# Optimization experiments

Measured on AMD Instinct MI355X. Metric: run time of the kernel, lower is better.

Reference implementation:

```python
import jax, jax.numpy as jnp
import numpy as np

N_EMBED = 384
N_HEAD = 6
HEAD_SIZE = N_EMBED // N_HEAD  # 64
LN_EPS = 1e-5


def setup_inputs() -> dict:
    key = jax.random.key(0)
    ks = jax.random.split(key, 12)
    B, T = 128, 256
    s_in = 1.0 / np.sqrt(N_EMBED)
    s_ff = 1.0 / np.sqrt(4 * N_EMBED)
    return {
        "x": jax.random.normal(ks[0], (B, T, N_EMBED), jnp.float32),
        "Wq": jax.random.normal(ks[1], (N_HEAD, N_EMBED, HEAD_SIZE), jnp.float32) * s_in,
        "Wk": jax.random.normal(ks[2], (N_HEAD, N_EMBED, HEAD_SIZE), jnp.float32) * s_in,
        "Wv": jax.random.normal(ks[3], (N_HEAD, N_EMBED, HEAD_SIZE), jnp.float32) * s_in,
        "Wproj": jax.random.normal(ks[4], (N_EMBED, N_EMBED), jnp.float32) * s_in,
        "bproj": jnp.zeros((N_EMBED,), jnp.float32),
        "W1": jax.random.normal(ks[5], (N_EMBED, 4 * N_EMBED), jnp.float32) * s_in,
        "b1": jnp.zeros((4 * N_EMBED,), jnp.float32),
        "W2": jax.random.normal(ks[6], (4 * N_EMBED, N_EMBED), jnp.float32) * s_ff,
        "b2": jnp.zeros((N_EMBED,), jnp.float32),
        "ln1_g": jnp.ones((N_EMBED,), jnp.float32),
        "ln1_b": jnp.zeros((N_EMBED,), jnp.float32),
        "ln2_g": jnp.ones((N_EMBED,), jnp.float32),
        "ln2_b": jnp.zeros((N_EMBED,), jnp.float32),
    }


def _layernorm(x, g, b):
    mu = jnp.mean(x, axis=-1, keepdims=True)
    var = jnp.mean(jnp.square(x - mu), axis=-1, keepdims=True)
    return (x - mu) * jax.lax.rsqrt(var + LN_EPS) * g + b


def _attention(xn, Wq, Wk, Wv, Wproj, bproj):
    B, T, C = xn.shape
    q = jnp.einsum("btc,hcd->bhtd", xn, Wq)
    k = jnp.einsum("btc,hcd->bhtd", xn, Wk)
    v = jnp.einsum("btc,hcd->bhtd", xn, Wv)
    # NOTE: original scales by C**-0.5 with C = n_embed (384), not head_size
    scores = jnp.einsum("bhtd,bhsd->bhts", q, k) * (C ** -0.5)
    causal = jnp.tril(jnp.ones((T, T), bool))
    scores = jnp.where(causal, scores, -jnp.inf)
    wei = jax.nn.softmax(scores, axis=-1)
    out = jnp.einsum("bhts,bhsd->bhtd", wei, v)
    out = out.transpose(0, 2, 1, 3).reshape(B, T, N_EMBED)  # concat heads
    return out @ Wproj + bproj


def reference(x, Wq, Wk, Wv, Wproj, bproj, W1, b1, W2, b2, ln1_g, ln1_b, ln2_g, ln2_b):
    x = x + _attention(_layernorm(x, ln1_g, ln1_b), Wq, Wk, Wv, Wproj, bproj)
    h = _layernorm(x, ln2_g, ln2_b)
    ff = jax.nn.relu(h @ W1 + b1) @ W2 + b2
    return x + ff
```

## Files before the change

### kernel.cpp

```cpp
#include <hip/hip_runtime.h>
#include <hip/hip_bf16.h>

typedef __hip_bfloat16 bf16;
typedef __attribute__((ext_vector_type(8))) short bf16x8;
typedef __attribute__((ext_vector_type(4))) float f32x4;

#define CEMB 384
#define NHEAD 6
#define HSZ 64
#define TSEQ 256
#define BATCH 128
#define MROWS (BATCH*TSEQ)
#define FDIM 1536
#define QSCALE 0.05103103630798288f
#define SMAX 8.0f

#define AS1 __attribute__((address_space(1)))
#define AS3 __attribute__((address_space(3)))
__device__ __forceinline__ void gload16(const void* g, void* l){
  __builtin_amdgcn_global_load_lds((const AS1 unsigned*)(g), (AS3 unsigned*)(l), 16, 0, 0);
}

__global__ __launch_bounds__(256) void ln_kernel(const float* __restrict__ x,
    const float* __restrict__ gam, const float* __restrict__ bet,
    bf16* __restrict__ y)
{
  const int row  = blockIdx.x*4 + (threadIdx.x>>6);
  const int lane = threadIdx.x & 63;
  const float* xr = x + (size_t)row*CEMB;
  float v[6]; float s = 0.f;
  #pragma unroll
  for (int i=0;i<6;i++){ v[i] = xr[lane + i*64]; s += v[i]; }
  #pragma unroll
  for (int m=1;m<64;m<<=1) s += __shfl_xor(s, m, 64);
  const float mu = s * (1.0f/CEMB);
  float qs = 0.f;
  #pragma unroll
  for (int i=0;i<6;i++){ v[i] -= mu; qs += v[i]*v[i]; }
  #pragma unroll
  for (int m=1;m<64;m<<=1) qs += __shfl_xor(qs, m, 64);
  const float rs = rsqrtf(qs*(1.0f/CEMB) + 1e-5f);
  bf16* yr = y + (size_t)row*CEMB;
  #pragma unroll
  for (int i=0;i<6;i++){
    int c = lane + i*64;
    yr[c] = __float2bfloat16(v[i]*rs*gam[c] + bet[c]);
  }
}

__global__ __launch_bounds__(256) void transpose_to_bf16(const float* __restrict__ src,
    bf16* __restrict__ dst, int K, int N)
{
  __shared__ float tile[32][33];
  const int n0 = blockIdx.x*32, k0 = blockIdx.y*32;
  src += (size_t)blockIdx.z*K*N;
  dst += (size_t)blockIdx.z*K*N;
  const int c = threadIdx.x & 31, r8 = threadIdx.x >> 5;
  #pragma unroll
  for (int i=0;i<4;i++)
    tile[r8 + i*8][c] = src[(size_t)(k0 + r8 + i*8)*N + n0 + c];
  __syncthreads();
  #pragma unroll
  for (int i=0;i<4;i++)
    dst[(size_t)(n0 + r8 + i*8)*K + k0 + c] = __float2bfloat16(tile[c][r8 + i*8]);
}

__global__ __launch_bounds__(256) void transpose_qkv(const float* __restrict__ Wq,
    const float* __restrict__ Wk, const float* __restrict__ Wv, bf16* __restrict__ dst)
{
  __shared__ float tile[32][33];
  const int z = blockIdx.z;
  const float* src = (z < 6) ? Wq : (z < 12 ? Wk : Wv);
  src += (size_t)(z % 6) * CEMB * HSZ;
  dst += (size_t)z * CEMB * HSZ;
  const int n0 = blockIdx.x*32, k0 = blockIdx.y*32;
  const int c = threadIdx.x & 31, r8 = threadIdx.x >> 5;
  #pragma unroll
  for (int i=0;i<4;i++)
    tile[r8 + i*8][c] = src[(size_t)(k0 + r8 + i*8)*HSZ + n0 + c];
  __syncthreads();
  #pragma unroll
  for (int i=0;i<4;i++)
    dst[(size_t)(n0 + r8 + i*8)*CEMB + k0 + c] = __float2bfloat16(tile[c][r8 + i*8]);
}

template<int EPI, int NREAL, int NPAD, int NK>
__global__ __launch_bounds__(512, 2) void gemm8p(
    const bf16* __restrict__ A, const bf16* __restrict__ BT,
    const float* __restrict__ bias, const float* __restrict__ resid,
    float* __restrict__ outf, bf16* __restrict__ outb0,
    bf16* __restrict__ outb1, bf16* __restrict__ outb2)
{
  constexpr int K = NK*64;
  constexpr int NT = NPAD/256;
  __shared__ char lds[131072];
  const int cpx = gridDim.x >> 3;
  const int wg  = (blockIdx.x & 7)*cpx + (blockIdx.x >> 3);
  const int bm = (wg / NT)*256, bn = (wg % NT)*256;
  const int t = threadIdx.x, lane = t & 63, wid = t >> 6;
  const int wm = wid >> 2, wn = wid & 3;
  const int g = lane >> 4, fr = lane & 15;
  const size_t rowb = (size_t)K*2;
  const int sblk = ((t&3) ^ ((t>>3)&3)) << 4;
  const int swz  = (g ^ ((fr>>1)&3)) << 4;
  f32x4 acc[8][4] = {};

  const char* Ag = (const char*)A  + (size_t)(bm + (t>>2))*rowb + sblk;
  const char* Bg = (const char*)BT + (size_t)(bn + (t>>2))*rowb + sblk;
  const size_t rstep = rowb*128;

  auto stg = [&](int X, int KH, int sl, int kt2){
    const char* src = (X ? Bg : Ag) + (size_t)kt2*128 + KH*64;
    char* dst = lds + X*65536 + (KH*2+sl)*16384 + wid*1024;
    gload16(src,         dst);
    gload16(src + rstep, dst + 8192);
  };
  auto rdA = [&](bf16x8* af, int sl, int MH, int KS){
    const char* p = lds + (KS*2+sl)*16384 + (wm*128 + MH*64 + fr)*64 + swz;
    #pragma unroll
    for (int mi=0;mi<4;mi++) af[mi] = *(const bf16x8*)(p + mi*1024);
  };
  auto rdB = [&](bf16x8* bq, int sl, int KS){
    const char* p = lds + 65536 + (KS*2+sl)*16384 + (wn*64 + fr)*64 + swz;
    #pragma unroll
    for (int nj=0;nj<4;nj++) bq[nj] = *(const bf16x8*)(p + nj*1024);
  };

#define MFMA16(MH) \
  __builtin_amdgcn_s_setprio(1); \
  _Pragma("unroll") \
  for (int mi=0;mi<4;mi++){ \
    _Pragma("unroll") \
    for (int nj=0;nj<4;nj++) \
      acc[(MH)*4+mi][nj] = __builtin_amdgcn_mfma_f32_16x16x32_bf16(af[mi], bq[nj], acc[(MH)*4+mi][nj], 0, 0, 0); \
  } \
  __builtin_amdgcn_s_setprio(0);

  stg(0,0,0,0); stg(1,0,0,0); stg(0,1,0,0); stg(1,1,0,0);
  asm volatile("s_waitcnt vmcnt(4)" ::: "memory");
  __builtin_amdgcn_s_barrier();

  #pragma unroll 1
  for (int kt=0; kt<NK; ++kt){
    const int sl = kt&1, sn = sl^1;
    const bool pf = (kt+1 < NK);
    bf16x8 af[4], bq[4];
    rdA(af, sl, 0, 0); rdB(bq, sl, 0);
    if (pf) stg(0,0,sn,kt+1);
    __builtin_amdgcn_s_barrier();
    asm volatile("s_waitcnt lgkmcnt(0)" ::: "memory");
    __builtin_amdgcn_sched_barrier(0);
    MFMA16(0)
    __builtin_amdgcn_s_barrier();
    rdA(af, sl, 1, 0);
    if (pf){ stg(1,0,sn,kt+1);
             asm volatile("s_waitcnt vmcnt(4)" ::: "memory"); }
    else     asm volatile("s_waitcnt vmcnt(0)" ::: "memory");
    __builtin_amdgcn_s_barrier();
    asm volatile("s_waitcnt lgkmcnt(0)" ::: "memory");
    __builtin_amdgcn_sched_barrier(0);
    MFMA16(1)
    __builtin_amdgcn_s_barrier();
    rdA(af, sl, 0, 1); rdB(bq, sl, 1);
    if (pf) stg(0,1,sn,kt+1);
    __builtin_amdgcn_s_barrier();
    asm volatile("s_waitcnt lgkmcnt(0)" ::: "memory");
    __builtin_amdgcn_sched_barrier(0);
    MFMA16(0)
    __builtin_amdgcn_s_barrier();
    rdA(af, sl, 1, 1);
    if (pf){ stg(1,1,sn,kt+1);
             asm volatile("s_waitcnt vmcnt(4)" ::: "memory"); }
    __builtin_amdgcn_s_barrier();
    asm volatile("s_waitcnt lgkmcnt(0)" ::: "memory");
    __builtin_amdgcn_sched_barrier(0);
    MFMA16(1)
    __builtin_amdgcn_s_barrier();
  }
#undef MFMA16

  #pragma unroll
  for (int mi=0;mi<8;mi++)
    #pragma unroll
    for (int nj=0;nj<4;nj++)
      #pragma unroll
      for (int e=0;e<4;e++){
        const int m = bm + wm*128 + mi*16 + 4*g + e;
        const int n = bn + wn*64 + nj*16 + fr;
        if (NPAD == NREAL || n < NREAL){
          const float vacc = acc[mi][nj][e];
          if constexpr (EPI==0){
            int sel = n/CEMB; int nn = n - sel*CEMB;
            int hh = nn>>6, dd = nn&63;
            int bb = m>>8,  tt = m&255;
            bf16 val = __float2bfloat16(sel==0 ? vacc * QSCALE : vacc);
            bf16* dst = sel==0 ? outb0 : (sel==1 ? outb1 : outb2);
            dst[((size_t)(bb*NHEAD + hh)*TSEQ + tt)*HSZ + dd] = val;
          } else if constexpr (EPI==1){
            outf[(size_t)m*NREAL + n] = vacc + bias[n] + resid[(size_t)m*NREAL + n];
          } else {
            float z = vacc + bias[n];
            outb0[(size_t)m*NREAL + n] = __float2bfloat16(z > 0.f ? z : 0.f);
          }
        }
      }
}

template<int EPI, int NN, int NK>
__global__ __launch_bounds__(512) void gemm3(
    const bf16* __restrict__ A, const bf16* __restrict__ BT,
    const float* __restrict__ bias, const float* __restrict__ resid,
    float* __restrict__ outf)
{
  constexpr int K = NK*32;
  constexpr int N = NN*128;
  __shared__ char lA[2][256*64];
  __shared__ char lB[2][128*64];
  const int cpx = gridDim.x >> 3;
  const int wg  = (blockIdx.x & 7)*cpx + (blockIdx.x >> 3);
  const int bm = (wg / NN)*256, bn = (wg % NN)*128;
  const int t = threadIdx.x, lane = t & 63, wid = t >> 6;
  const int wr = (wid>>1)*64, wc = (wid&1)*64;
  const int g = lane >> 4, fr = lane & 15;
  const size_t rowK2 = (size_t)K*2;
  f32x4 acc[4][4] = {};

  auto stage = [&](int buf, int kt){
    const size_t ko = (size_t)kt*64;
    #pragma unroll
    for (int i=0;i<2;i++){
      int slot = t + i*512;
      int row = slot>>2, blk = slot&3;
      gload16((const char*)A + (size_t)(bm+row)*rowK2 + ko + ((blk ^ ((row>>1)&3))<<4),
              lA[buf] + slot*16);
    }
    {
      int row = t>>2, blk = t&3;
      gload16((const char*)BT + (size_t)(bn+row)*rowK2 + ko + ((blk ^ ((row>>1)&3))<<4),
              lB[buf] + t*16);
    }
  };

  stage(0, 0);
  __syncthreads();
  int cur = 0;
  #pragma unroll 1
  for (int kt=0; kt<NK; ++kt){
    if (kt+1 < NK) stage(cur^1, kt+1);
    bf16x8 af[4], bq[4];
    #pragma unroll
    for (int mi=0;mi<4;mi++){
      int row = wr + mi*16 + fr;
      af[mi] = *(const bf16x8*)(lA[cur] + row*64 + ((g ^ ((row>>1)&3))<<4));
    }
    #pragma unroll
    for (int nj=0;nj<4;nj++){
      int row = wc + nj*16 + fr;
      bq[nj] = *(const bf16x8*)(lB[cur] + row*64 + ((g ^ ((row>>1)&3))<<4));
    }
    __builtin_amdgcn_s_setprio(1);
    #pragma unroll
    for (int mi=0;mi<4;mi++)
      #pragma unroll
      for (int nj=0;nj<4;nj++)
        acc[mi][nj] = __builtin_amdgcn_mfma_f32_16x16x32_bf16(af[mi], bq[nj], acc[mi][nj], 0, 0, 0);
    __builtin_amdgcn_s_setprio(0);
    __syncthreads();
    cur ^= 1;
  }
  #pragma unroll
  for (int mi=0;mi<4;mi++)
    #pragma unroll
    for (int nj=0;nj<4;nj++)
      #pragma unroll
      for (int e=0;e<4;e++){
        const int m = bm + wr + mi*16 + 4*g + e;
        const int n = bn + wc + nj*16 + fr;
        outf[(size_t)m*N + n] = acc[mi][nj][e] + bias[n] + resid[(size_t)m*N + n];
      }
}

__global__ __launch_bounds__(256) void attn_kernel(
    const bf16* __restrict__ q, const bf16* __restrict__ k,
    const bf16* __restrict__ v, bf16* __restrict__ out)
{
  __shared__ char kt_lds[64*128];
  __shared__ char vt_lds[80*128];
  __shared__ char p_lds[4][64*128];
  const int bh = blockIdx.x;
  const int bidx = bh / NHEAD, hidx = bh - bidx*NHEAD;
  const int t = threadIdx.x, lane = t & 63, w = t >> 6;
  const int g = lane >> 4, fr = lane & 15;
  const int lrow = lane >> 3;
  const int scol = ((lane & 7) ^ lrow) << 4;
  const size_t base = (size_t)bh * TSEQ * HSZ;

  if (t < 128){
    unsigned int ones2 = 0x3F803F80u;
    uint4 vv;
    if ((t>>3) == 0) vv = uint4{ones2, ones2, ones2, ones2};
    else             vv = uint4{0u, 0u, 0u, 0u};
    *(uint4*)(vt_lds + (64 + (t>>3))*128 + (t&7)*16) = vv;
  }

  bf16x8 qf[4][2];
  #pragma unroll
  for (int mi=0;mi<4;mi++)
    #pragma unroll
    for (int ks=0;ks<2;ks++)
      qf[mi][ks] = *(const bf16x8*)(q + base + (size_t)(w*64 + mi*16 + fr)*HSZ + ks*32 + g*8);

  f32x4 of[4][5] = {};

  for (int j=0;j<4;j++){
    __syncthreads();
    #pragma unroll
    for (int i=0;i<2;i++){
      int r0 = w*16 + i*8;
      gload16((const char*)(k + base + (size_t)(j*64 + r0 + lrow)*HSZ) + scol,
              kt_lds + r0*128);
    }
    #pragma unroll
    for (int i=0;i<2;i++){
      int chunk = t + i*256, r = chunk>>3, c = chunk&7;
      uint4 vv = *(const uint4*)(v + base + (size_t)(j*64 + r)*HSZ + c*8);
      const unsigned short* pv = (const unsigned short*)&vv;
      #pragma unroll
      for (int u=0;u<8;u++)
        *(unsigned short*)(vt_lds + (c*8+u)*128 + ((((r>>3) ^ u ^ c)&7)<<4) + (r&7)*2) = pv[u];
    }
    __syncthreads();
    if (j <= w){
      f32x4 sa[4][4] = {};
      #pragma unroll
      for (int ks=0;ks<2;ks++){
        bf16x8 kf[4];
        #pragma unroll
        for (int nj=0;nj<4;nj++)
          kf[nj] = *(const bf16x8*)(kt_lds + (nj*16+fr)*128 + (((ks*4+g)*16) ^ ((fr&7)<<4)));
        __builtin_amdgcn_s_setprio(1);
        #pragma unroll
        for (int mi=0;mi<4;mi++)
          #pragma unroll
          for (int nj=0;nj<4;nj++)
            sa[mi][nj] = __builtin_amdgcn_mfma_f32_16x16x32_bf16(qf[mi][ks], kf[nj], sa[mi][nj], 0, 0, 0);
        __builtin_amdgcn_s_setprio(0);
      }
      if (j == w){
        #pragma unroll
        for (int mi=0;mi<4;mi++)
          #pragma unroll
          for (int nj=0;nj<4;nj++)
            #pragma unroll
            for (int e=0;e<4;e++)
              if (nj*16 + fr > mi*16 + 4*g + e) sa[mi][nj][e] = -1e30f;
      }
      char* pl = p_lds[w];
      #pragma unroll
      for (int mi=0;mi<4;mi++)
        #pragma unroll
        for (int nj=0;nj<4;nj++)
          #pragma unroll
          for (int e=0;e<4;e++){
            int row = mi*16 + 4*g + e, col = nj*16 + fr;
            float p = __expf(sa[mi][nj][e] - SMAX);
            *(bf16*)(pl + row*128 + (((col>>3) ^ (row&7))<<4) + (col&7)*2) =
                __float2bfloat16(p);
          }
      #pragma unroll
      for (int ks=0;ks<2;ks++){
        bf16x8 pa[4], vf[5];
        #pragma unroll
        for (int mi=0;mi<4;mi++)
          pa[mi] = *(const bf16x8*)(pl + (mi*16+fr)*128 + (((ks*4+g)*16) ^ ((fr&7)<<4)));
        #pragma unroll
        for (int nd=0;nd<5;nd++){
          int d = nd*16 + fr;
          vf[nd] = *(const bf16x8*)(vt_lds + d*128 +
                   ((((ks*4+g) ^ (d&7) ^ ((d>>3)&7))&7)<<4));
        }
        __builtin_amdgcn_s_setprio(1);
        #pragma unroll
        for (int mi=0;mi<4;mi++)
          #pragma unroll
          for (int nd=0;nd<5;nd++)
            of[mi][nd] = __builtin_amdgcn_mfma_f32_16x16x32_bf16(pa[mi], vf[nd], of[mi][nd], 0, 0, 0);
        __builtin_amdgcn_s_setprio(0);
      }
    }
  }
  #pragma unroll
  for (int mi=0;mi<4;mi++){
    float rl[4];
    #pragma unroll
    for (int e=0;e<4;e++){
      float l = __shfl(of[mi][4][e], (int)(lane & 48), 64);
      rl[e] = 1.0f / l;
    }
    #pragma unroll
    for (int nd=0;nd<4;nd++)
      #pragma unroll
      for (int e=0;e<4;e++){
        int row = w*64 + mi*16 + 4*g + e;
        int d = nd*16 + fr;
        out[(size_t)(bidx*TSEQ + row)*CEMB + hidx*HSZ + d] =
            __float2bfloat16(of[mi][nd][e] * rl[e]);
      }
  }
}

extern "C" void kernel_launch(void* const* d_in, const int* in_sizes, int n_in,
                              void* d_out, int out_size, void* d_ws, size_t ws_size,
                              hipStream_t stream)
{
  const float* x     = (const float*)d_in[0];
  const float* Wq    = (const float*)d_in[1];
  const float* Wk    = (const float*)d_in[2];
  const float* Wv    = (const float*)d_in[3];
  const float* Wproj = (const float*)d_in[4];
  const float* bproj = (const float*)d_in[5];
  const float* W1    = (const float*)d_in[6];
  const float* b1    = (const float*)d_in[7];
  const float* W2    = (const float*)d_in[8];
  const float* b2    = (const float*)d_in[9];
  const float* ln1g  = (const float*)d_in[10];
  const float* ln1b  = (const float*)d_in[11];
  const float* ln2g  = (const float*)d_in[12];
  const float* ln2b  = (const float*)d_in[13];

  char* ws = (char*)d_ws;
  const size_t SA = (size_t)MROWS*CEMB*2;
  bf16* xn1    = (bf16*)(ws + 0*SA);
  bf16* qb     = (bf16*)(ws + 1*SA);
  bf16* kbuf   = (bf16*)(ws + 2*SA);
  bf16* vb     = (bf16*)(ws + 3*SA);
  bf16* attn_o = (bf16*)(ws + 0*SA);
  bf16* act    = (bf16*)(ws + 0*SA);
  bf16* hb     = (bf16*)(ws + 4*SA);
  float* x1    = (float*)(ws + 5*SA);
  char* wb     = ws + 5*SA + (size_t)MROWS*CEMB*4;
  bf16* qkvT   = (bf16*)wb;
  bf16* projT  = (bf16*)(wb + (size_t)1280*384*2);
  bf16* w1T    = (bf16*)(wb + (size_t)(1280+512)*384*2);
  bf16* w2T    = (bf16*)(wb + (size_t)(1280+512+1536)*384*2);

  dim3 blk(256), blk5(512);
  transpose_qkv<<<dim3(2,12,18), blk, 0, stream>>>(Wq, Wk, Wv, qkvT);
  transpose_to_bf16<<<dim3(12,12,1), blk, 0, stream>>>(Wproj, projT, CEMB, CEMB);
  transpose_to_bf16<<<dim3(48,12,1), blk, 0, stream>>>(W1,    w1T,   CEMB, FDIM);
  transpose_to_bf16<<<dim3(12,48,1), blk, 0, stream>>>(W2,    w2T,   FDIM, CEMB);

  ln_kernel<<<dim3(MROWS/4), blk, 0, stream>>>(x, ln1g, ln1b, xn1);
  gemm8p<0,1152,1280,6><<<dim3(640), blk5, 0, stream>>>(xn1, qkvT, nullptr, nullptr,
                                                        nullptr, qb, kbuf, vb);
  attn_kernel<<<dim3(768), blk, 0, stream>>>(qb, kbuf, vb, attn_o);
  gemm8p<1,384,512,6><<<dim3(256), blk5, 0, stream>>>(attn_o, projT, bproj, x,
                                                      x1, nullptr, nullptr, nullptr);
  ln_kernel<<<dim3(MROWS/4), blk, 0, stream>>>(x1, ln2g, ln2b, hb);
  gemm8p<2,1536,1536,6><<<dim3(768), blk5, 0, stream>>>(hb, w1T, b1, nullptr,
                                                        nullptr, act, nullptr, nullptr);
  gemm3<3,3,48><<<dim3(384), blk5, 0, stream>>>(act, w2T, b2, x1, (float*)d_out);
}
```

Before: 276.6 us.

## Swap GEMM kernels per stage and store residual intermediate in bf16

```diff
diff --git a/kernel.cpp b/kernel.cpp
--- a/kernel.cpp
+++ b/kernel.cpp
@@ -20,6 +20,9 @@
 __device__ __forceinline__ void gload16(const void* g, void* l){
   __builtin_amdgcn_global_load_lds((const AS1 unsigned*)(g), (AS3 unsigned*)(l), 16, 0, 0);
 }
+__device__ __forceinline__ float b2f(unsigned short u){
+  unsigned int xi = ((unsigned int)u)<<16; float f; __builtin_memcpy(&f,&xi,4); return f;
+}
 
 __global__ __launch_bounds__(256) void ln_kernel(const float* __restrict__ x,
     const float* __restrict__ gam, const float* __restrict__ bet,
@@ -46,6 +49,39 @@
     int c = lane + i*64;
     yr[c] = __float2bfloat16(v[i]*rs*gam[c] + bet[c]);
   }
+}
+
+__global__ __launch_bounds__(256) void ln_kernel_b(const bf16* __restrict__ x,
+    const float* __restrict__ gam, const float* __restrict__ bet,
+    bf16* __restrict__ y)
+{
+  const int row  = blockIdx.x*4 + (threadIdx.x>>6);
+  const int lane = threadIdx.x & 63;
+  const ushort2* xr = (const ushort2*)(x + (size_t)row*CEMB);
+  float v[6]; float s = 0.f;
+  #pragma unroll
+  for (int i=0;i<3;i++){
+    ushort2 u = xr[lane + i*64];
+    v[2*i]   = b2f(u.x); v[2*i+1] = b2f(u.y);
+    s += v[2*i] + v[2*i+1];
+  }
+  #pragma unroll
+  for (int m=1;m<64;m<<=1) s += __shfl_xor(s, m, 64);
+  const float mu = s * (1.0f/CEMB);
+  float qs = 0.f;
+  #pragma unroll
+  for (int i=0;i<6;i++){ v[i] -= mu; qs += v[i]*v[i]; }
+  #pragma unroll
+  for (int m=1;m<64;m<<=1) qs += __shfl_xor(qs, m, 64);
+  const float rs = rsqrtf(qs*(1.0f/CEMB) + 1e-5f);
+  bf16* yr = y + (size_t)row*CEMB;
+  #pragma unroll
+  for (int i=0;i<3;i++)
+    #pragma unroll
+    for (int j=0;j<2;j++){
+      int c = (lane + i*64)*2 + j;
+      yr[c] = __float2bfloat16(v[2*i+j]*rs*gam[c] + bet[c]);
+    }
 }
 
 __global__ __launch_bounds__(256) void transpose_to_bf16(const float* __restrict__ src,
@@ -84,12 +120,114 @@
     dst[(size_t)(n0 + r8 + i*8)*CEMB + k0 + c] = __float2bfloat16(tile[c][r8 + i*8]);
 }
 
-template<int EPI, int NREAL, int NPAD, int NK>
-__global__ __launch_bounds__(512, 2) void gemm8p(
+template<int EPI, int NN, int NK>
+__global__ __launch_bounds__(512) void gemm2(
     const bf16* __restrict__ A, const bf16* __restrict__ BT,
     const float* __restrict__ bias, const float* __restrict__ resid,
     float* __restrict__ outf, bf16* __restrict__ outb0,
     bf16* __restrict__ outb1, bf16* __restrict__ outb2)
+{
+  constexpr int K = NK*32;
+  constexpr int N = NN*128;
+  __shared__ char lA[2][256*64];
+  __shared__ char lB[2][128*64];
+  const int cpx = gridDim.x >> 3;
+  const int wg  = (blockIdx.x & 7)*cpx + (blockIdx.x >> 3);
+  const int bm = (wg / NN)*256, bn = (wg % NN)*128;
+  const int t = threadIdx.x, lane = t & 63, wid = t >> 6;
+  const int wr = (wid>>1)*64, wc = (wid&1)*64;
+  const int g = lane >> 4, fr = lane & 15;
+  const size_t rowK2 = (size_t)K*2;
+  f32x4 acc[4][4] = {};
+
+  auto stage = [&](int buf, int kt){
+    const size_t ko = (size_t)kt*64;
+    #pragma unroll
+    for (int i=0;i<2;i++){
+      int slot = t + i*512;
+      int row = slot>>2, blk = slot&3;
+      gload16((const char*)A + (size_t)(bm+row)*rowK2 + ko + ((blk ^ ((row>>1)&3))<<4),
+              lA[buf] + slot*16);
+    }
+    {
+      int row = t>>2, blk = t&3;
+      gload16((const char*)BT + (size_t)(bn+row)*rowK2 + ko + ((blk ^ ((row>>1)&3))<<4),
+              lB[buf] + t*16);
+    }
+  };
+
+  stage(0, 0);
+  __syncthreads();
+  int cur = 0;
+  #pragma unroll 1
+  for (int kt=0; kt<NK; ++kt){
+    if (kt+1 < NK) stage(cur^1, kt+1);
+    bf16x8 af[4], bq[4];
+    #pragma unroll
+    for (int mi=0;mi<4;mi++){
+      int row = wr + mi*16 + fr;
+      af[mi] = *(const bf16x8*)(lA[cur] + row*64 + ((g ^ ((row>>1)&3))<<4));
+    }
+    #pragma unroll
+    for (int nj=0;nj<4;nj++){
+      int row = wc + nj*16 + fr;
+      bq[nj] = *(const bf16x8*)(lB[cur] + row*64 + ((g ^ ((row>>1)&3))<<4));
+    }
+    __builtin_amdgcn_s_setprio(1);
+    #pragma unroll
+    for (int mi=0;mi<4;mi++)
+      #pragma unroll
+      for (int nj=0;nj<4;nj++)
+        acc[mi][nj] = __builtin_amdgcn_mfma_f32_16x16x32_bf16(af[mi], bq[nj], acc[mi][nj], 0, 0, 0);
+    __builtin_amdgcn_s_setprio(0);
+    __syncthreads();
+    cur ^= 1;
+  }
+
+  if constexpr (EPI==0){
+    const int sel = bn/CEMB;
+    bf16* dst = sel==0 ? outb0 : (sel==1 ? outb1 : outb2);
+    const float sc = sel==0 ? QSCALE : 1.0f;
+    const int nb = bn - sel*CEMB;
+    #pragma unroll
+    for (int nj=0;nj<4;nj++){
+      const int nn = nb + wc + nj*16 + fr;
+      const int hh = nn>>6, dd = nn&63;
+      #pragma unroll
+      for (int mi=0;mi<4;mi++){
+        const int m0 = bm + wr + mi*16 + 4*g;
+        const int bb = m0>>8, tt0 = m0&255;
+        bf16* p = dst + ((size_t)(bb*NHEAD + hh)*TSEQ + tt0)*HSZ + dd;
+        #pragma unroll
+        for (int e=0;e<4;e++)
+          p[(size_t)e*HSZ] = __float2bfloat16(acc[mi][nj][e]*sc);
+      }
+    }
+  } else {
+    #pragma unroll
+    for (int mi=0;mi<4;mi++)
+      #pragma unroll
+      for (int nj=0;nj<4;nj++)
+        #pragma unroll
+        for (int e=0;e<4;e++){
+          const int m = bm + wr + mi*16 + 4*g + e;
+          const int n = bn + wc + nj*16 + fr;
+          const float vacc = acc[mi][nj][e];
+          if constexpr (EPI==1){
+            outb0[(size_t)m*N + n] = __float2bfloat16(vacc + bias[n] + resid[(size_t)m*N + n]);
+          } else {
+            float z = vacc + bias[n];
+            outb0[(size_t)m*N + n] = __float2bfloat16(z > 0.f ? z : 0.f);
+          }
+        }
+  }
+}
+
+template<int EPI, int NREAL, int NPAD, int NK>
+__global__ __launch_bounds__(512, 2) void gemm8p(
+    const bf16* __restrict__ A, const bf16* __restrict__ BT,
+    const float* __restrict__ bias, const bf16* __restrict__ residb,
+    float* __restrict__ outf)
 {
   constexpr int K = NK*64;
   constexpr int NT = NPAD/256;
@@ -189,94 +327,9 @@
         const int n = bn + wn*64 + nj*16 + fr;
         if (NPAD == NREAL || n < NREAL){
           const float vacc = acc[mi][nj][e];
-          if constexpr (EPI==0){
-            int sel = n/CEMB; int nn = n - sel*CEMB;
-            int hh = nn>>6, dd = nn&63;
-            int bb = m>>8,  tt = m&255;
-            bf16 val = __float2bfloat16(sel==0 ? vacc * QSCALE : vacc);
-            bf16* dst = sel==0 ? outb0 : (sel==1 ? outb1 : outb2);
-            dst[((size_t)(bb*NHEAD + hh)*TSEQ + tt)*HSZ + dd] = val;
-          } else if constexpr (EPI==1){
-            outf[(size_t)m*NREAL + n] = vacc + bias[n] + resid[(size_t)m*NREAL + n];
-          } else {
-            float z = vacc + bias[n];
-            outb0[(size_t)m*NREAL + n] = __float2bfloat16(z > 0.f ? z : 0.f);
-          }
+          outf[(size_t)m*NREAL + n] = vacc + bias[n] +
+              b2f(*(const unsigned short*)&residb[(size_t)m*NREAL + n]);
         }
-      }
-}
-
-template<int EPI, int NN, int NK>
-__global__ __launch_bounds__(512) void gemm3(
-    const bf16* __restrict__ A, const bf16* __restrict__ BT,
-    const float* __restrict__ bias, const float* __restrict__ resid,
-    float* __restrict__ outf)
-{
-  constexpr int K = NK*32;
-  constexpr int N = NN*128;
-  __shared__ char lA[2][256*64];
-  __shared__ char lB[2][128*64];
-  const int cpx = gridDim.x >> 3;
-  const int wg  = (blockIdx.x & 7)*cpx + (blockIdx.x >> 3);
-  const int bm = (wg / NN)*256, bn = (wg % NN)*128;
-  const int t = threadIdx.x, lane = t & 63, wid = t >> 6;
-  const int wr = (wid>>1)*64, wc = (wid&1)*64;
-  const int g = lane >> 4, fr = lane & 15;
-  const size_t rowK2 = (size_t)K*2;
-  f32x4 acc[4][4] = {};
-
-  auto stage = [&](int buf, int kt){
-    const size_t ko = (size_t)kt*64;
-    #pragma unroll
-    for (int i=0;i<2;i++){
-      int slot = t + i*512;
-      int row = slot>>2, blk = slot&3;
-      gload16((const char*)A + (size_t)(bm+row)*rowK2 + ko + ((blk ^ ((row>>1)&3))<<4),
-              lA[buf] + slot*16);
-    }
-    {
-      int row = t>>2, blk = t&3;
-      gload16((const char*)BT + (size_t)(bn+row)*rowK2 + ko + ((blk ^ ((row>>1)&3))<<4),
-              lB[buf] + t*16);
-    }
-  };
-
-  stage(0, 0);
-  __syncthreads();
-  int cur = 0;
-  #pragma unroll 1
-  for (int kt=0; kt<NK; ++kt){
-    if (kt+1 < NK) stage(cur^1, kt+1);
-    bf16x8 af[4], bq[4];
-    #pragma unroll
-    for (int mi=0;mi<4;mi++){
-      int row = wr + mi*16 + fr;
-      af[mi] = *(const bf16x8*)(lA[cur] + row*64 + ((g ^ ((row>>1)&3))<<4));
-    }
-    #pragma unroll
-    for (int nj=0;nj<4;nj++){
-      int row = wc + nj*16 + fr;
-      bq[nj] = *(const bf16x8*)(lB[cur] + row*64 + ((g ^ ((row>>1)&3))<<4));
-    }
-    __builtin_amdgcn_s_setprio(1);
-    #pragma unroll
-    for (int mi=0;mi<4;mi++)
-      #pragma unroll
-      for (int nj=0;nj<4;nj++)
-        acc[mi][nj] = __builtin_amdgcn_mfma_f32_16x16x32_bf16(af[mi], bq[nj], acc[mi][nj], 0, 0, 0);
-    __builtin_amdgcn_s_setprio(0);
-    __syncthreads();
-    cur ^= 1;
-  }
-  #pragma unroll
-  for (int mi=0;mi<4;mi++)
-    #pragma unroll
-    for (int nj=0;nj<4;nj++)
-      #pragma unroll
-      for (int e=0;e<4;e++){
-        const int m = bm + wr + mi*16 + 4*g + e;
-        const int n = bn + wc + nj*16 + fr;
-        outf[(size_t)m*N + n] = acc[mi][nj][e] + bias[n] + resid[(size_t)m*N + n];
       }
 }
 
@@ -437,12 +490,12 @@
   bf16* attn_o = (bf16*)(ws + 0*SA);
   bf16* act    = (bf16*)(ws + 0*SA);
   bf16* hb     = (bf16*)(ws + 4*SA);
-  float* x1    = (float*)(ws + 5*SA);
+  bf16* x1b    = (bf16*)(ws + 5*SA);
   char* wb     = ws + 5*SA + (size_t)MROWS*CEMB*4;
   bf16* qkvT   = (bf16*)wb;
-  bf16* projT  = (bf16*)(wb + (size_t)1280*384*2);
-  bf16* w1T    = (bf16*)(wb + (size_t)(1280+512)*384*2);
-  bf16* w2T    = (bf16*)(wb + (size_t)(1280+512+1536)*384*2);
+  bf16* projT  = (bf16*)(wb + (size_t)1152*384*2);
+  bf16* w1T    = (bf16*)(wb + (size_t)(1152+384)*384*2);
+  bf16* w2T    = (bf16*)(wb + (size_t)(1152+384+1536)*384*2);
 
   dim3 blk(256), blk5(512);
   transpose_qkv<<<dim3(2,12,18), blk, 0, stream>>>(Wq, Wk, Wv, qkvT);
@@ -451,13 +504,13 @@
   transpose_to_bf16<<<dim3(12,48,1), blk, 0, stream>>>(W2,    w2T,   FDIM, CEMB);
 
   ln_kernel<<<dim3(MROWS/4), blk, 0, stream>>>(x, ln1g, ln1b, xn1);
-  gemm8p<0,1152,1280,6><<<dim3(640), blk5, 0, stream>>>(xn1, qkvT, nullptr, nullptr,
-                                                        nullptr, qb, kbuf, vb);
+  gemm2<0,9,12><<<dim3(1152), blk5, 0, stream>>>(xn1, qkvT, nullptr, nullptr,
+                                                 nullptr, qb, kbuf, vb);
   attn_kernel<<<dim3(768), blk, 0, stream>>>(qb, kbuf, vb, attn_o);
-  gemm8p<1,384,512,6><<<dim3(256), blk5, 0, stream>>>(attn_o, projT, bproj, x,
-                                                      x1, nullptr, nullptr, nullptr);
-  ln_kernel<<<dim3(MROWS/4), blk, 0, stream>>>(x1, ln2g, ln2b, hb);
-  gemm8p<2,1536,1536,6><<<dim3(768), blk5, 0, stream>>>(hb, w1T, b1, nullptr,
-                                                        nullptr, act, nullptr, nullptr);
-  gemm3<3,3,48><<<dim3(384), blk5, 0, stream>>>(act, w2T, b2, x1, (float*)d_out);
-}
+  gemm2<1,3,12><<<dim3(384), blk5, 0, stream>>>(attn_o, projT, bproj, x,
+                                                nullptr, x1b, nullptr, nullptr);
+  ln_kernel_b<<<dim3(MROWS/4), blk, 0, stream>>>(x1b, ln2g, ln2b, hb);
+  gemm2<2,12,12><<<dim3(1536), blk5, 0, stream>>>(hb, w1T, b1, nullptr,
+                                                  nullptr, act, nullptr, nullptr);
+  gemm8p<3,384,512,24><<<dim3(256), blk5, 0, stream>>>(act, w2T, b2, x1b, (float*)d_out);
+}
```

New measurement: 261.5 us. 1.06x faster.
